# Kernel optimization log

Measured on AMD Instinct MI355X. Metric: run time of the kernel, lower is better.

The kernel has to match this reference:

```python
import jax, jax.numpy as jnp
import numpy as np
from jax import lax

EPS = 1e-5

@jax.custom_vjp
def binarize(x):
    return jnp.sign(x)

def _bin_fwd(x):
    return jnp.sign(x), x

def _bin_bwd(x, g):
    # straight-through estimator: pass grad where |x| <= 1
    return (g * (jnp.abs(x) <= 1.0).astype(g.dtype),)

binarize.defvjp(_bin_fwd, _bin_bwd)


def bconv(x, w, stride=1, pad=0):
    # BinarizeConv2d: sign-binarize both activations and weights, dense conv
    return lax.conv_general_dilated(
        binarize(x), binarize(w),
        window_strides=(stride, stride),
        padding=[(pad, pad), (pad, pad)],
        dimension_numbers=('NCHW', 'OIHW', 'NCHW'))


def bn(x, gamma, beta):
    # training-mode batch norm (grad enabled in torch forward): batch stats over (N,H,W)
    mean = x.mean(axis=(0, 2, 3), keepdims=True)
    var = ((x - mean) ** 2).mean(axis=(0, 2, 3), keepdims=True)
    return gamma * (x - mean) * lax.rsqrt(var + EPS) + beta


def hardtanh(x):
    return jnp.clip(x, -1.0, 1.0)


def setup_inputs() -> dict:
    key = jax.random.key(0)
    ks = jax.random.split(key, 4)
    N, Cin, H, W = 64, 256, 56, 56
    P = 64  # planes; expansion*planes == Cin -> identity shortcut
    return {
        'x':  jax.random.normal(ks[0], (N, Cin, H, W), dtype=jnp.float32),
        'w1': jax.random.normal(ks[1], (P, Cin, 1, 1), dtype=jnp.float32),
        'w2': jax.random.normal(ks[2], (P, P, 3, 3), dtype=jnp.float32),
        'w3': jax.random.normal(ks[3], (Cin, P, 1, 1), dtype=jnp.float32),
        'g1': jnp.ones((1, P, 1, 1), jnp.float32),
        'b1': jnp.zeros((1, P, 1, 1), jnp.float32),
        'g2': jnp.ones((1, P, 1, 1), jnp.float32),
        'b2': jnp.zeros((1, P, 1, 1), jnp.float32),
        'g3': jnp.ones((1, Cin, 1, 1), jnp.float32),
        'b3': jnp.zeros((1, Cin, 1, 1), jnp.float32),
    }


def reference(x, w1, w2, w3, g1, b1, g2, b2, g3, b3):
    out = hardtanh(bn(bconv(x, w1), g1, b1))                 # 1x1 binconv + BN + hardtanh
    out = hardtanh(bn(bconv(out, w2, stride=1, pad=1), g2, b2))  # 3x3 binconv + BN + hardtanh
    out = bn(bconv(out, w3), g3, b3)                          # 1x1 binconv + BN
    out = out + x                                             # identity shortcut
    return hardtanh(out)
```

## Files before the change

### kernel.cpp

```cpp
#include <hip/hip_runtime.h>
#include <stdint.h>
#include <math.h>

typedef unsigned long long u64;
typedef long long ll;

#define H_    56
#define W_    56
#define HW_   3136
#define N_    64
#define C_    256
#define P_    64
#define NPIX_ 200704
#define BN_EPS 1e-5

__global__ __launch_bounds__(256) void pack_weights_k(
    const float* __restrict__ w1, const float* __restrict__ w2,
    const float* __restrict__ w3,
    u64* __restrict__ ws1, u64* __restrict__ wn1,
    u64* __restrict__ ws2, u64* __restrict__ wn2, int* __restrict__ b2,
    u64* __restrict__ ws3, u64* __restrict__ wn3, int* __restrict__ b3) {
  int t = blockIdx.x * 256 + threadIdx.x;
  if (t < 64) {
    int co = t;
    for (int ch = 0; ch < 4; ++ch) {
      u64 s = 0, n = 0;
      for (int j = 0; j < 64; ++j) {
        float v = w1[co * 256 + ch * 64 + j];
        s |= ((u64)(v < 0.f)) << j;
        n |= ((u64)(v != 0.f)) << j;
      }
      ws1[co * 4 + ch] = s; wn1[co * 4 + ch] = n;
    }
  } else if (t < 64 + 576) {
    int idx = t - 64, co = idx / 9, tap = idx % 9;
    u64 s = 0, n = 0;
    for (int ci = 0; ci < 64; ++ci) {
      float v = w2[(co * 64 + ci) * 9 + tap];
      s |= ((u64)(v < 0.f)) << ci;
      n |= ((u64)(v != 0.f)) << ci;
    }
    ws2[idx] = s; wn2[idx] = n; b2[idx] = __popcll(n);
  } else if (t < 64 + 576 + 256) {
    int co = t - 640;
    u64 s = 0, n = 0;
    for (int ci = 0; ci < 64; ++ci) {
      float v = w3[co * 64 + ci];
      s |= ((u64)(v < 0.f)) << ci;
      n |= ((u64)(v != 0.f)) << ci;
    }
    ws3[co] = s; wn3[co] = n; b3[co] = __popcll(n);
  }
}

__global__ __launch_bounds__(256) void fused1_k(
    const float* __restrict__ x,
    const u64* __restrict__ ws1, const u64* __restrict__ wn1,
    short* __restrict__ y1, u64* __restrict__ gsum, u64* __restrict__ gsq) {
  __shared__ u64 lws[256], lwn[256];
  __shared__ int ssum[64], ssq[64];
  int tid = threadIdx.x;
  lws[tid] = ws1[tid]; lwn[tid] = wn1[tid];
  if (tid < 64) { ssum[tid] = 0; ssq[tid] = 0; }
  __syncthreads();

  int p = blockIdx.x * 256 + tid;
  int n = p / HW_, hw = p % HW_;
  const float* xb = x + (size_t)n * (C_ * HW_) + hw;
  u64 s[4], nb[4];
  #pragma unroll
  for (int ch = 0; ch < 4; ++ch) {
    u64 sv = 0, nv = 0;
    #pragma unroll
    for (int j = 0; j < 64; ++j) {
      float v = xb[(size_t)((ch * 64 + j) * HW_)];
      sv |= ((u64)(v < 0.f)) << j;
      nv |= ((u64)(v != 0.f)) << j;
    }
    s[ch] = sv; nb[ch] = nv;
  }

  int lane = tid & 63;
  for (int co = 0; co < 64; ++co) {
    int acc = 0;
    #pragma unroll
    for (int ch = 0; ch < 4; ++ch) {
      u64 v = nb[ch] & lwn[co * 4 + ch];
      u64 a = ~(s[ch] ^ lws[co * 4 + ch]) & v;
      acc += 2 * __popcll(a) - __popcll(v);
    }
    y1[(size_t)co * NPIX_ + p] = (short)acc;
    int rs = acc, rq = acc * acc;
    #pragma unroll
    for (int m = 32; m; m >>= 1) {
      rs += __shfl_xor(rs, m, 64);
      rq += __shfl_xor(rq, m, 64);
    }
    if (lane == 0) { atomicAdd(&ssum[co], rs); atomicAdd(&ssq[co], rq); }
  }
  __syncthreads();
  if (tid < 64) {
    atomicAdd(&gsum[tid], (u64)(ll)ssum[tid]);
    atomicAdd(&gsq[tid],  (u64)(ll)ssq[tid]);
  }
}

__global__ __launch_bounds__(256) void binpack_k(
    const short* __restrict__ y,
    const u64* __restrict__ gsum, const u64* __restrict__ gsq,
    const float* __restrict__ gamma, const float* __restrict__ beta,
    u64* __restrict__ pout) {
  __shared__ double tsc[64], tsh[64];
  int tid = threadIdx.x;
  if (tid < 64) {
    double S = (double)(ll)gsum[tid], Q = (double)(ll)gsq[tid];
    double mean = S / (double)NPIX_;
    double var  = Q / (double)NPIX_ - mean * mean;
    double inv  = 1.0 / sqrt(var + BN_EPS);
    double sc   = (double)gamma[tid] * inv;
    tsc[tid] = sc;
    tsh[tid] = (double)beta[tid] - mean * sc;
  }
  __syncthreads();
  int p = blockIdx.x * 256 + tid;
  u64 m = 0;
  #pragma unroll 8
  for (int co = 0; co < 64; ++co) {
    int v = (int)y[(size_t)co * NPIX_ + p];
    m |= ((u64)(tsc[co] * (double)v + tsh[co] < 0.0)) << co;
  }
  pout[p] = m;
}

__global__ __launch_bounds__(256) void conv2_k(
    const u64* __restrict__ p1,
    const u64* __restrict__ ws2, const u64* __restrict__ wn2,
    const int* __restrict__ b2,
    short* __restrict__ y2, u64* __restrict__ gsum, u64* __restrict__ gsq) {
  __shared__ u64 lws[576], lwn[576];
  __shared__ int lb[576];
  __shared__ int ssum[64], ssq[64];
  int tid = threadIdx.x;
  for (int j = tid; j < 576; j += 256) { lws[j] = ws2[j]; lwn[j] = wn2[j]; lb[j] = b2[j]; }
  if (tid < 64) { ssum[tid] = 0; ssq[tid] = 0; }
  __syncthreads();

  int p = blockIdx.x * 256 + tid;
  int n = p / HW_, hw = p % HW_, h = hw / W_, w = hw % W_;
  u64 tv[9]; bool ok[9];
  #pragma unroll
  for (int dh = -1; dh <= 1; ++dh)
    #pragma unroll
    for (int dw = -1; dw <= 1; ++dw) {
      int k = (dh + 1) * 3 + (dw + 1);
      int h2 = h + dh, w2c = w + dw;
      bool v = (h2 >= 0) & (h2 < H_) & (w2c >= 0) & (w2c < W_);
      ok[k] = v;
      tv[k] = v ? p1[n * HW_ + h2 * W_ + w2c] : 0ULL;
    }

  int lane = tid & 63;
  for (int co = 0; co < 64; ++co) {
    int acc = 0;
    #pragma unroll
    for (int k = 0; k < 9; ++k) {
      int wi = co * 9 + k;
      u64 a = ~(tv[k] ^ lws[wi]) & lwn[wi];
      int d = 2 * __popcll(a) - lb[wi];
      acc += ok[k] ? d : 0;
    }
    y2[(size_t)co * NPIX_ + p] = (short)acc;
    int rs = acc, rq = acc * acc;
    #pragma unroll
    for (int m = 32; m; m >>= 1) {
      rs += __shfl_xor(rs, m, 64);
      rq += __shfl_xor(rq, m, 64);
    }
    if (lane == 0) { atomicAdd(&ssum[co], rs); atomicAdd(&ssq[co], rq); }
  }
  __syncthreads();
  if (tid < 64) {
    atomicAdd(&gsum[tid], (u64)(ll)ssum[tid]);
    atomicAdd(&gsq[tid],  (u64)(ll)ssq[tid]);
  }
}

__global__ __launch_bounds__(256) void conv3_stats_k(
    const u64* __restrict__ p2,
    const u64* __restrict__ ws3, const u64* __restrict__ wn3,
    const int* __restrict__ b3,
    u64* __restrict__ gsum, u64* __restrict__ gsq) {
  int t = threadIdx.x;
  u64 s3 = ws3[t], n3 = wn3[t];
  int bb = b3[t];
  int s = 0, q = 0;
  int base = blockIdx.x * 512;
  #pragma unroll 4
  for (int i = 0; i < 512; ++i) {
    u64 m = p2[base + i];
    int yv = 2 * __popcll(~(m ^ s3) & n3) - bb;
    s += yv; q += yv * yv;
  }
  atomicAdd(&gsum[t], (u64)(ll)s);
  atomicAdd(&gsq[t],  (u64)(ll)q);
}

__global__ __launch_bounds__(256) void final_k(
    const float* __restrict__ x, const u64* __restrict__ p2,
    const u64* __restrict__ ws3, const u64* __restrict__ wn3,
    const int* __restrict__ b3,
    const u64* __restrict__ gsum, const u64* __restrict__ gsq,
    const float* __restrict__ gamma, const float* __restrict__ beta,
    float* __restrict__ out) {
  __shared__ float fsc[2], fsh[2];
  size_t base = (size_t)blockIdx.x * 1024;
  size_t r0 = base / HW_;
  if (threadIdx.x < 2) {
    int c = (int)((r0 + threadIdx.x) % C_);
    double S = (double)(ll)gsum[c], Q = (double)(ll)gsq[c];
    double mean = S / (double)NPIX_;
    double var  = Q / (double)NPIX_ - mean * mean;
    double inv  = 1.0 / sqrt(var + BN_EPS);
    double sc   = (double)gamma[c] * inv;
    fsc[threadIdx.x] = (float)sc;
    fsh[threadIdx.x] = (float)((double)beta[c] - mean * sc);
  }
  __syncthreads();

  size_t idx = base + (size_t)threadIdx.x * 4;
  size_t lin = idx / HW_;
  int rr = (int)(lin - r0);
  int co = (int)(lin % C_);
  int nn = (int)(lin / C_);
  int hw = (int)(idx % HW_);
  int pb = nn * HW_ + hw;
  u64 s3 = ws3[co], n3 = wn3[co];
  int bb = b3[co];
  float sc = fsc[rr], sh = fsh[rr];
  float4 xv = *(const float4*)(x + idx);
  float4 ov;
  int y0 = 2 * __popcll(~(p2[pb + 0] ^ s3) & n3) - bb;
  int y1 = 2 * __popcll(~(p2[pb + 1] ^ s3) & n3) - bb;
  int y2 = 2 * __popcll(~(p2[pb + 2] ^ s3) & n3) - bb;
  int y3 = 2 * __popcll(~(p2[pb + 3] ^ s3) & n3) - bb;
  ov.x = fminf(fmaxf(sc * (float)y0 + sh + xv.x, -1.f), 1.f);
  ov.y = fminf(fmaxf(sc * (float)y1 + sh + xv.y, -1.f), 1.f);
  ov.z = fminf(fmaxf(sc * (float)y2 + sh + xv.z, -1.f), 1.f);
  ov.w = fminf(fmaxf(sc * (float)y3 + sh + xv.w, -1.f), 1.f);
  *(float4*)(out + idx) = ov;
}

extern "C" void kernel_launch(void* const* d_in, const int* in_sizes, int n_in,
                              void* d_out, int out_size, void* d_ws, size_t ws_size,
                              hipStream_t stream) {
  const float* x  = (const float*)d_in[0];
  const float* w1 = (const float*)d_in[1];
  const float* w2 = (const float*)d_in[2];
  const float* w3 = (const float*)d_in[3];
  const float* g1 = (const float*)d_in[4];
  const float* b1 = (const float*)d_in[5];
  const float* g2 = (const float*)d_in[6];
  const float* b2 = (const float*)d_in[7];
  const float* g3 = (const float*)d_in[8];
  const float* b3 = (const float*)d_in[9];
  float* out = (float*)d_out;

  char* base = (char*)d_ws;
  size_t off = 0;
  auto alloc = [&](size_t bytes) -> char* {
    char* p = base + off;
    off = (off + bytes + 255) & ~(size_t)255;
    return p;
  };
  short* y1b = (short*)alloc((size_t)NPIX_ * 64 * 2);
  u64* p1   = (u64*)alloc((size_t)NPIX_ * 8);
  u64* p2   = (u64*)alloc((size_t)NPIX_ * 8);
  u64* ws1  = (u64*)alloc(256 * 8);
  u64* wn1  = (u64*)alloc(256 * 8);
  u64* ws2  = (u64*)alloc(576 * 8);
  u64* wn2  = (u64*)alloc(576 * 8);
  int* bb2  = (int*)alloc(576 * 4);
  u64* ws3  = (u64*)alloc(256 * 8);
  u64* wn3  = (u64*)alloc(256 * 8);
  int* bb3  = (int*)alloc(256 * 4);
  char* stats = alloc(768 * 8);
  u64* sum1 = (u64*)stats;          u64* sq1 = sum1 + 64;
  u64* sum2 = sq1 + 64;             u64* sq2 = sum2 + 64;
  u64* sum3 = sq2 + 64;             u64* sq3 = sum3 + 256;
  (void)ws_size; (void)n_in; (void)in_sizes; (void)out_size;

  hipMemsetAsync(stats, 0, 768 * 8, stream);

  pack_weights_k<<<4, 256, 0, stream>>>(w1, w2, w3, ws1, wn1, ws2, wn2, bb2,
                                        ws3, wn3, bb3);

  fused1_k<<<784, 256, 0, stream>>>(x, ws1, wn1, y1b, sum1, sq1);
  binpack_k<<<784, 256, 0, stream>>>(y1b, sum1, sq1, g1, b1, p1);

  conv2_k<<<784, 256, 0, stream>>>(p1, ws2, wn2, bb2, y1b, sum2, sq2);
  binpack_k<<<784, 256, 0, stream>>>(y1b, sum2, sq2, g2, b2, p2);

  conv3_stats_k<<<392, 256, 0, stream>>>(p2, ws3, wn3, bb3, sum3, sq3);

  final_k<<<50176, 256, 0, stream>>>(x, p2, ws3, wn3, bb3, sum3, sq3, g3, b3,
                                     out);
}
```

Measured before the change: 617.2 us.

## Recompute binary convs in a second pass instead of storing int16 intermediates

The first-layer sign packing is split out into its own kernel, which writes packed sign and nonzero bitplanes of x. Conv1 and conv2 now run twice: a stats-only pass, then a pass that recomputes the conv and binarizes it against an integer threshold derived from the BN stats. This removes the 25 MB short intermediate buffers and the separate binpack kernels. Threads are remapped so each lane owns an output channel with its weights held in registers, and each wave walks over pixels, building the packed words with ballots. The trade is twice the popcount work in exchange for far less memory traffic, plus a 13 MB packed-x buffer that the two conv1 passes re-read.

```diff
diff --git a/kernel.cpp b/kernel.cpp
--- a/kernel.cpp
+++ b/kernel.cpp
@@ -3,6 +3,7 @@
 #include <math.h>
 
 typedef unsigned long long u64;
+typedef unsigned int u32;
 typedef long long ll;
 
 #define H_    56
@@ -53,51 +54,87 @@
   }
 }
 
-__global__ __launch_bounds__(256) void fused1_k(
-    const float* __restrict__ x,
+__device__ inline void bn_thresh(u64 S_, u64 Q_, float g, float b,
+                                 int* A, int* X) {
+  double S = (double)(ll)S_, Q = (double)(ll)Q_;
+  double mean = S / (double)NPIX_;
+  double var  = Q / (double)NPIX_ - mean * mean;
+  double sc   = (double)g / sqrt(var + BN_EPS);
+  double sh   = (double)b - mean * sc;
+  if (sc > 0.0) {
+    double t = -sh / sc;
+    t = fmin(fmax(t, -1.0e8), 1.0e8);
+    *A = (int)ceil(t); *X = 0;
+  } else if (sc < 0.0) {
+    double t = -sh / sc;
+    t = fmin(fmax(t, -1.0e8), 1.0e8);
+    *A = (int)floor(t) + 1; *X = 1;
+  } else {
+    *A = (int)0x80000000; *X = (sh < 0.0) ? 1 : 0;
+  }
+}
+
+__global__ __launch_bounds__(64) void pack_x_k(
+    const float* __restrict__ x, u64* __restrict__ xs, u64* __restrict__ xn) {
+  int t = blockIdx.x * 64 + threadIdx.x;
+  int n = t / 784;
+  int qw = t - n * 784;
+  const float* xb = x + (size_t)n * (C_ * HW_) + qw * 4;
+  size_t p = (size_t)t * 4;
+  for (int q = 0; q < 4; ++q) {
+    u64 s0 = 0, s1 = 0, s2 = 0, s3 = 0, n0 = 0, n1 = 0, n2 = 0, n3 = 0;
+    #pragma unroll 8
+    for (int j = 0; j < 64; ++j) {
+      float4 v = *(const float4*)(xb + (size_t)(q * 64 + j) * HW_);
+      u64 bit = 1ull << j;
+      if (v.x <  0.f) s0 |= bit;
+      if (v.x != 0.f) n0 |= bit;
+      if (v.y <  0.f) s1 |= bit;
+      if (v.y != 0.f) n1 |= bit;
+      if (v.z <  0.f) s2 |= bit;
+      if (v.z != 0.f) n2 |= bit;
+      if (v.w <  0.f) s3 |= bit;
+      if (v.w != 0.f) n3 |= bit;
+    }
+    u64* os = xs + (size_t)q * NPIX_ + p;
+    u64* on = xn + (size_t)q * NPIX_ + p;
+    ulonglong2 a, b2v, c, d;
+    a.x = s0; a.y = s1; b2v.x = s2; b2v.y = s3;
+    c.x = n0; c.y = n1; d.x = n2; d.y = n3;
+    *(ulonglong2*)(os)     = a;
+    *(ulonglong2*)(os + 2) = b2v;
+    *(ulonglong2*)(on)     = c;
+    *(ulonglong2*)(on + 2) = d;
+  }
+}
+
+__global__ __launch_bounds__(256) void conv1_stats_k(
+    const u64* __restrict__ xs, const u64* __restrict__ xn,
     const u64* __restrict__ ws1, const u64* __restrict__ wn1,
-    short* __restrict__ y1, u64* __restrict__ gsum, u64* __restrict__ gsq) {
-  __shared__ u64 lws[256], lwn[256];
+    u64* __restrict__ gsum, u64* __restrict__ gsq) {
   __shared__ int ssum[64], ssq[64];
-  int tid = threadIdx.x;
-  lws[tid] = ws1[tid]; lwn[tid] = wn1[tid];
+  int tid = threadIdx.x, co = tid & 63, wv = tid >> 6;
   if (tid < 64) { ssum[tid] = 0; ssq[tid] = 0; }
+  u64 wS[4], wN[4];
+  #pragma unroll
+  for (int q = 0; q < 4; ++q) { wS[q] = ws1[co * 4 + q]; wN[q] = wn1[co * 4 + q]; }
   __syncthreads();
-
-  int p = blockIdx.x * 256 + tid;
-  int n = p / HW_, hw = p % HW_;
-  const float* xb = x + (size_t)n * (C_ * HW_) + hw;
-  u64 s[4], nb[4];
-  #pragma unroll
-  for (int ch = 0; ch < 4; ++ch) {
-    u64 sv = 0, nv = 0;
-    #pragma unroll
-    for (int j = 0; j < 64; ++j) {
-      float v = xb[(size_t)((ch * 64 + j) * HW_)];
-      sv |= ((u64)(v < 0.f)) << j;
-      nv |= ((u64)(v != 0.f)) << j;
-    }
-    s[ch] = sv; nb[ch] = nv;
-  }
-
-  int lane = tid & 63;
-  for (int co = 0; co < 64; ++co) {
+  int pbase = (blockIdx.x * 4 + wv) * 64;
+  int s = 0, qq = 0;
+  for (int i = 0; i < 64; ++i) {
+    int p = pbase + i;
     int acc = 0;
     #pragma unroll
-    for (int ch = 0; ch < 4; ++ch) {
-      u64 v = nb[ch] & lwn[co * 4 + ch];
-      u64 a = ~(s[ch] ^ lws[co * 4 + ch]) & v;
+    for (int q = 0; q < 4; ++q) {
+      u64 xv = xs[(size_t)q * NPIX_ + p];
+      u64 nv = xn[(size_t)q * NPIX_ + p];
+      u64 v = nv & wN[q];
+      u64 a = ~(xv ^ wS[q]) & v;
       acc += 2 * __popcll(a) - __popcll(v);
     }
-    y1[(size_t)co * NPIX_ + p] = (short)acc;
-    int rs = acc, rq = acc * acc;
-    #pragma unroll
-    for (int m = 32; m; m >>= 1) {
-      rs += __shfl_xor(rs, m, 64);
-      rq += __shfl_xor(rq, m, 64);
-    }
-    if (lane == 0) { atomicAdd(&ssum[co], rs); atomicAdd(&ssq[co], rq); }
-  }
+    s += acc; qq += acc * acc;
+  }
+  atomicAdd(&ssum[co], s); atomicAdd(&ssq[co], qq);
   __syncthreads();
   if (tid < 64) {
     atomicAdd(&gsum[tid], (u64)(ll)ssum[tid]);
@@ -105,84 +142,150 @@
   }
 }
 
-__global__ __launch_bounds__(256) void binpack_k(
-    const short* __restrict__ y,
+__global__ __launch_bounds__(256) void bin1_k(
+    const u64* __restrict__ xs, const u64* __restrict__ xn,
+    const u64* __restrict__ ws1, const u64* __restrict__ wn1,
     const u64* __restrict__ gsum, const u64* __restrict__ gsq,
     const float* __restrict__ gamma, const float* __restrict__ beta,
     u64* __restrict__ pout) {
-  __shared__ double tsc[64], tsh[64];
-  int tid = threadIdx.x;
-  if (tid < 64) {
-    double S = (double)(ll)gsum[tid], Q = (double)(ll)gsq[tid];
-    double mean = S / (double)NPIX_;
-    double var  = Q / (double)NPIX_ - mean * mean;
-    double inv  = 1.0 / sqrt(var + BN_EPS);
-    double sc   = (double)gamma[tid] * inv;
-    tsc[tid] = sc;
-    tsh[tid] = (double)beta[tid] - mean * sc;
-  }
-  __syncthreads();
-  int p = blockIdx.x * 256 + tid;
-  u64 m = 0;
-  #pragma unroll 8
-  for (int co = 0; co < 64; ++co) {
-    int v = (int)y[(size_t)co * NPIX_ + p];
-    m |= ((u64)(tsc[co] * (double)v + tsh[co] < 0.0)) << co;
-  }
-  pout[p] = m;
-}
-
-__global__ __launch_bounds__(256) void conv2_k(
-    const u64* __restrict__ p1,
-    const u64* __restrict__ ws2, const u64* __restrict__ wn2,
-    const int* __restrict__ b2,
-    short* __restrict__ y2, u64* __restrict__ gsum, u64* __restrict__ gsq) {
-  __shared__ u64 lws[576], lwn[576];
-  __shared__ int lb[576];
-  __shared__ int ssum[64], ssq[64];
-  int tid = threadIdx.x;
-  for (int j = tid; j < 576; j += 256) { lws[j] = ws2[j]; lwn[j] = wn2[j]; lb[j] = b2[j]; }
-  if (tid < 64) { ssum[tid] = 0; ssq[tid] = 0; }
-  __syncthreads();
-
-  int p = blockIdx.x * 256 + tid;
-  int n = p / HW_, hw = p % HW_, h = hw / W_, w = hw % W_;
-  u64 tv[9]; bool ok[9];
+  int tid = threadIdx.x, co = tid & 63, wv = tid >> 6;
+  u64 wS[4], wN[4];
   #pragma unroll
-  for (int dh = -1; dh <= 1; ++dh)
-    #pragma unroll
-    for (int dw = -1; dw <= 1; ++dw) {
-      int k = (dh + 1) * 3 + (dw + 1);
-      int h2 = h + dh, w2c = w + dw;
-      bool v = (h2 >= 0) & (h2 < H_) & (w2c >= 0) & (w2c < W_);
-      ok[k] = v;
-      tv[k] = v ? p1[n * HW_ + h2 * W_ + w2c] : 0ULL;
-    }
-
-  int lane = tid & 63;
-  for (int co = 0; co < 64; ++co) {
+  for (int q = 0; q < 4; ++q) { wS[q] = ws1[co * 4 + q]; wN[q] = wn1[co * 4 + q]; }
+  int A, X;
+  bn_thresh(gsum[co], gsq[co], gamma[co], beta[co], &A, &X);
+  int pbase = (blockIdx.x * 4 + wv) * 64;
+  u64 mw = 0;
+  for (int i = 0; i < 64; ++i) {
+    int p = pbase + i;
     int acc = 0;
     #pragma unroll
-    for (int k = 0; k < 9; ++k) {
-      int wi = co * 9 + k;
-      u64 a = ~(tv[k] ^ lws[wi]) & lwn[wi];
-      int d = 2 * __popcll(a) - lb[wi];
-      acc += ok[k] ? d : 0;
-    }
-    y2[(size_t)co * NPIX_ + p] = (short)acc;
-    int rs = acc, rq = acc * acc;
-    #pragma unroll
-    for (int m = 32; m; m >>= 1) {
-      rs += __shfl_xor(rs, m, 64);
-      rq += __shfl_xor(rq, m, 64);
-    }
-    if (lane == 0) { atomicAdd(&ssum[co], rs); atomicAdd(&ssq[co], rq); }
-  }
+    for (int q = 0; q < 4; ++q) {
+      u64 xv = xs[(size_t)q * NPIX_ + p];
+      u64 nv = xn[(size_t)q * NPIX_ + p];
+      u64 v = nv & wN[q];
+      u64 a = ~(xv ^ wS[q]) & v;
+      acc += 2 * __popcll(a) - __popcll(v);
+    }
+    u64 bal = __ballot((acc < A) ^ X);
+    mw = (co == i) ? bal : mw;
+  }
+  pout[pbase + co] = mw;
+}
+
+__device__ inline int conv2_tap(u64 t, u64 ws, u64 wn, int b) {
+  return 2 * __popcll(~(t ^ ws) & wn) - b;
+}
+
+__device__ inline int conv2_px_edge(const u64* rowp, int w, int hm, int hp,
+                                    const u64* wS, const u64* wN,
+                                    const int* wB) {
+  int wm = (w > 0), wp = (w < W_ - 1);
+  int acc = 0;
+  if (hm & wm) acc += conv2_tap(rowp[w - W_ - 1], wS[0], wN[0], wB[0]);
+  if (hm)      acc += conv2_tap(rowp[w - W_    ], wS[1], wN[1], wB[1]);
+  if (hm & wp) acc += conv2_tap(rowp[w - W_ + 1], wS[2], wN[2], wB[2]);
+  if (wm)      acc += conv2_tap(rowp[w - 1     ], wS[3], wN[3], wB[3]);
+  acc += conv2_tap(rowp[w], wS[4], wN[4], wB[4]);
+  if (wp)      acc += conv2_tap(rowp[w + 1     ], wS[5], wN[5], wB[5]);
+  if (hp & wm) acc += conv2_tap(rowp[w + W_ - 1], wS[6], wN[6], wB[6]);
+  if (hp)      acc += conv2_tap(rowp[w + W_    ], wS[7], wN[7], wB[7]);
+  if (hp & wp) acc += conv2_tap(rowp[w + W_ + 1], wS[8], wN[8], wB[8]);
+  return acc;
+}
+
+__device__ inline int conv2_px_fast(const u64* c, const u64* wS,
+                                    const u64* wN, int Bs) {
+  int P = 0;
+  P += __popcll(~(c[-W_ - 1] ^ wS[0]) & wN[0]);
+  P += __popcll(~(c[-W_    ] ^ wS[1]) & wN[1]);
+  P += __popcll(~(c[-W_ + 1] ^ wS[2]) & wN[2]);
+  P += __popcll(~(c[-1     ] ^ wS[3]) & wN[3]);
+  P += __popcll(~(c[0      ] ^ wS[4]) & wN[4]);
+  P += __popcll(~(c[1      ] ^ wS[5]) & wN[5]);
+  P += __popcll(~(c[W_ - 1 ] ^ wS[6]) & wN[6]);
+  P += __popcll(~(c[W_     ] ^ wS[7]) & wN[7]);
+  P += __popcll(~(c[W_ + 1 ] ^ wS[8]) & wN[8]);
+  return 2 * P - Bs;
+}
+
+__global__ __launch_bounds__(256) void conv2_stats_k(
+    const u64* __restrict__ p1, const u64* __restrict__ ws2,
+    const u64* __restrict__ wn2,
+    u64* __restrict__ gsum, u64* __restrict__ gsq) {
+  __shared__ int ssum[64], ssq[64];
+  int tid = threadIdx.x, co = tid & 63, wv = tid >> 6;
+  if (tid < 64) { ssum[tid] = 0; ssq[tid] = 0; }
+  u64 wS[9], wN[9]; int wB[9]; int Bs = 0;
+  #pragma unroll
+  for (int k = 0; k < 9; ++k) {
+    wS[k] = ws2[co * 9 + k]; wN[k] = wn2[co * 9 + k];
+    wB[k] = __popcll(wN[k]); Bs += wB[k];
+  }
+  __syncthreads();
+  int row = blockIdx.x * 4 + wv;
+  int n = row / H_, h = row - n * H_;
+  const u64* rowp = p1 + (size_t)n * HW_ + h * W_;
+  int hm = (h > 0), hp = (h < H_ - 1);
+  int s = 0, q = 0;
+  if (hm & hp) {
+    { int a = conv2_px_edge(rowp, 0, 1, 1, wS, wN, wB); s += a; q += a * a; }
+    for (int w = 1; w < W_ - 1; ++w) {
+      int a = conv2_px_fast(rowp + w, wS, wN, Bs);
+      s += a; q += a * a;
+    }
+    { int a = conv2_px_edge(rowp, W_ - 1, 1, 1, wS, wN, wB); s += a; q += a * a; }
+  } else {
+    for (int w = 0; w < W_; ++w) {
+      int a = conv2_px_edge(rowp, w, hm, hp, wS, wN, wB);
+      s += a; q += a * a;
+    }
+  }
+  atomicAdd(&ssum[co], s); atomicAdd(&ssq[co], q);
   __syncthreads();
   if (tid < 64) {
     atomicAdd(&gsum[tid], (u64)(ll)ssum[tid]);
     atomicAdd(&gsq[tid],  (u64)(ll)ssq[tid]);
   }
+}
+
+__global__ __launch_bounds__(256) void bin2_k(
+    const u64* __restrict__ p1, const u64* __restrict__ ws2,
+    const u64* __restrict__ wn2,
+    const u64* __restrict__ gsum, const u64* __restrict__ gsq,
+    const float* __restrict__ gamma, const float* __restrict__ beta,
+    u64* __restrict__ pout) {
+  int tid = threadIdx.x, co = tid & 63, wv = tid >> 6;
+  u64 wS[9], wN[9]; int wB[9]; int Bs = 0;
+  #pragma unroll
+  for (int k = 0; k < 9; ++k) {
+    wS[k] = ws2[co * 9 + k]; wN[k] = wn2[co * 9 + k];
+    wB[k] = __popcll(wN[k]); Bs += wB[k];
+  }
+  int A, X;
+  bn_thresh(gsum[co], gsq[co], gamma[co], beta[co], &A, &X);
+  int row = blockIdx.x * 4 + wv;
+  int n = row / H_, h = row - n * H_;
+  const u64* rowp = p1 + (size_t)n * HW_ + h * W_;
+  u64* orow = pout + (size_t)n * HW_ + h * W_;
+  int hm = (h > 0), hp = (h < H_ - 1);
+  u64 mw = 0;
+  if (hm & hp) {
+    { int a = conv2_px_edge(rowp, 0, 1, 1, wS, wN, wB);
+      u64 bal = __ballot((a < A) ^ X); mw = (co == 0) ? bal : mw; }
+    for (int w = 1; w < W_ - 1; ++w) {
+      int a = conv2_px_fast(rowp + w, wS, wN, Bs);
+      u64 bal = __ballot((a < A) ^ X); mw = (co == w) ? bal : mw;
+    }
+    { int a = conv2_px_edge(rowp, W_ - 1, 1, 1, wS, wN, wB);
+      u64 bal = __ballot((a < A) ^ X); mw = (co == W_ - 1) ? bal : mw; }
+  } else {
+    for (int w = 0; w < W_; ++w) {
+      int a = conv2_px_edge(rowp, w, hm, hp, wS, wN, wB);
+      u64 bal = __ballot((a < A) ^ X); mw = (co == w) ? bal : mw;
+    }
+  }
+  if (co < W_) orow[co] = mw;
 }
 
 __global__ __launch_bounds__(256) void conv3_stats_k(
@@ -272,7 +375,8 @@
     off = (off + bytes + 255) & ~(size_t)255;
     return p;
   };
-  short* y1b = (short*)alloc((size_t)NPIX_ * 64 * 2);
+  u64* xs   = (u64*)alloc((size_t)NPIX_ * 4 * 8);
+  u64* xnz  = (u64*)alloc((size_t)NPIX_ * 4 * 8);
   u64* p1   = (u64*)alloc((size_t)NPIX_ * 8);
   u64* p2   = (u64*)alloc((size_t)NPIX_ * 8);
   u64* ws1  = (u64*)alloc(256 * 8);
@@ -294,11 +398,13 @@
   pack_weights_k<<<4, 256, 0, stream>>>(w1, w2, w3, ws1, wn1, ws2, wn2, bb2,
                                         ws3, wn3, bb3);
 
-  fused1_k<<<784, 256, 0, stream>>>(x, ws1, wn1, y1b, sum1, sq1);
-  binpack_k<<<784, 256, 0, stream>>>(y1b, sum1, sq1, g1, b1, p1);
-
-  conv2_k<<<784, 256, 0, stream>>>(p1, ws2, wn2, bb2, y1b, sum2, sq2);
-  binpack_k<<<784, 256, 0, stream>>>(y1b, sum2, sq2, g2, b2, p2);
+  pack_x_k<<<784, 64, 0, stream>>>(x, xs, xnz);
+
+  conv1_stats_k<<<784, 256, 0, stream>>>(xs, xnz, ws1, wn1, sum1, sq1);
+  bin1_k<<<784, 256, 0, stream>>>(xs, xnz, ws1, wn1, sum1, sq1, g1, b1, p1);
+
+  conv2_stats_k<<<896, 256, 0, stream>>>(p1, ws2, wn2, sum2, sq2);
+  bin2_k<<<896, 256, 0, stream>>>(p1, ws2, wn2, sum2, sq2, g2, b2, p2);
 
   conv3_stats_k<<<392, 256, 0, stream>>>(p2, ws3, wn3, bb3, sum3, sq3);
 
```

After: 716.2 us. 16.1% more time.

## Recompute binary convs in two passes instead of storing int16 intermediates

Applied to the files above, without the earlier changes.

Packs the input sign and nonzero bitmasks once in a separate kernel. Conv1 and conv2 then each run twice: a stats pass and a recompute pass that turns the BN affine into an integer threshold and builds the packed output with wave ballots. This drops the 25 MB int16 intermediate write and reread and the separate binpack kernels. Conv2 now stages input rows in shared memory, maps threads to output channels, and special-cases the borders, while conv3 stats also stage p2 in shared memory. The cost is doing the popcount work twice and extra pack buffers.

```diff
diff --git a/kernel.cpp b/kernel.cpp
--- a/kernel.cpp
+++ b/kernel.cpp
@@ -53,135 +53,204 @@
   }
 }
 
-__global__ __launch_bounds__(256) void fused1_k(
-    const float* __restrict__ x,
+__device__ inline void bn_thresh(u64 S_, u64 Q_, float g, float b,
+                                 int* A, int* X) {
+  double S = (double)(ll)S_, Q = (double)(ll)Q_;
+  double mean = S / (double)NPIX_;
+  double var  = Q / (double)NPIX_ - mean * mean;
+  double sc   = (double)g / sqrt(var + BN_EPS);
+  double sh   = (double)b - mean * sc;
+  if (sc > 0.0) {
+    double t = -sh / sc;
+    t = fmin(fmax(t, -1.0e8), 1.0e8);
+    *A = (int)ceil(t); *X = 0;
+  } else if (sc < 0.0) {
+    double t = -sh / sc;
+    t = fmin(fmax(t, -1.0e8), 1.0e8);
+    *A = (int)floor(t) + 1; *X = 1;
+  } else {
+    *A = (int)0x80000000; *X = (sh < 0.0) ? 1 : 0;
+  }
+}
+
+__global__ __launch_bounds__(256) void pack_x_k(
+    const float* __restrict__ x, u64* __restrict__ xs, u64* __restrict__ xn) {
+  int t = blockIdx.x * 256 + threadIdx.x;
+  int n = t / 1568;
+  int pw = (t - n * 1568) * 2;
+  const float* xb = x + (size_t)n * (C_ * HW_) + pw;
+  size_t p = (size_t)t * 2;
+  for (int q = 0; q < 4; ++q) {
+    u64 s0 = 0, s1 = 0, n0 = 0, n1 = 0;
+    #pragma unroll 16
+    for (int j = 0; j < 64; ++j) {
+      float2 v = *(const float2*)(xb + (size_t)(q * 64 + j) * HW_);
+      u64 bit = 1ull << j;
+      if (v.x <  0.f) s0 |= bit;
+      if (v.x != 0.f) n0 |= bit;
+      if (v.y <  0.f) s1 |= bit;
+      if (v.y != 0.f) n1 |= bit;
+    }
+    ulonglong2 sv; sv.x = s0; sv.y = s1;
+    ulonglong2 nv; nv.x = n0; nv.y = n1;
+    *(ulonglong2*)(xs + (size_t)q * NPIX_ + p) = sv;
+    *(ulonglong2*)(xn + (size_t)q * NPIX_ + p) = nv;
+  }
+}
+
+template<int MODE>
+__global__ __launch_bounds__(256) void conv1_k(
+    const u64* __restrict__ xs, const u64* __restrict__ xn,
     const u64* __restrict__ ws1, const u64* __restrict__ wn1,
-    short* __restrict__ y1, u64* __restrict__ gsum, u64* __restrict__ gsq) {
-  __shared__ u64 lws[256], lwn[256];
+    u64* __restrict__ gsum, u64* __restrict__ gsq,
+    const float* __restrict__ gamma, const float* __restrict__ beta,
+    u64* __restrict__ pout) {
+  __shared__ ulonglong2 tile[4][256];
   __shared__ int ssum[64], ssq[64];
-  int tid = threadIdx.x;
-  lws[tid] = ws1[tid]; lwn[tid] = wn1[tid];
-  if (tid < 64) { ssum[tid] = 0; ssq[tid] = 0; }
+  int tid = threadIdx.x, co = tid & 63, wv = tid >> 6;
+  int base = blockIdx.x * 256;
+  #pragma unroll
+  for (int q = 0; q < 4; ++q) {
+    ulonglong2 v;
+    v.x = xs[(size_t)q * NPIX_ + base + tid];
+    v.y = xn[(size_t)q * NPIX_ + base + tid];
+    tile[q][tid] = v;
+  }
+  if (MODE == 0 && tid < 64) { ssum[tid] = 0; ssq[tid] = 0; }
+  u64 wS[4], wN[4];
+  #pragma unroll
+  for (int q = 0; q < 4; ++q) { wS[q] = ws1[co * 4 + q]; wN[q] = wn1[co * 4 + q]; }
+  int A = 0, X = 0;
+  if (MODE == 1) bn_thresh(gsum[co], gsq[co], gamma[co], beta[co], &A, &X);
   __syncthreads();
-
-  int p = blockIdx.x * 256 + tid;
-  int n = p / HW_, hw = p % HW_;
-  const float* xb = x + (size_t)n * (C_ * HW_) + hw;
-  u64 s[4], nb[4];
-  #pragma unroll
-  for (int ch = 0; ch < 4; ++ch) {
-    u64 sv = 0, nv = 0;
-    #pragma unroll
-    for (int j = 0; j < 64; ++j) {
-      float v = xb[(size_t)((ch * 64 + j) * HW_)];
-      sv |= ((u64)(v < 0.f)) << j;
-      nv |= ((u64)(v != 0.f)) << j;
-    }
-    s[ch] = sv; nb[ch] = nv;
-  }
-
-  int lane = tid & 63;
-  for (int co = 0; co < 64; ++co) {
+  int s = 0, qq = 0;
+  u64 mw = 0;
+  #pragma unroll 2
+  for (int i = 0; i < 64; ++i) {
+    int px = wv * 64 + i;
     int acc = 0;
     #pragma unroll
-    for (int ch = 0; ch < 4; ++ch) {
-      u64 v = nb[ch] & lwn[co * 4 + ch];
-      u64 a = ~(s[ch] ^ lws[co * 4 + ch]) & v;
+    for (int q = 0; q < 4; ++q) {
+      ulonglong2 t2 = tile[q][px];
+      u64 v = t2.y & wN[q];
+      u64 a = ~(t2.x ^ wS[q]) & v;
       acc += 2 * __popcll(a) - __popcll(v);
     }
-    y1[(size_t)co * NPIX_ + p] = (short)acc;
-    int rs = acc, rq = acc * acc;
-    #pragma unroll
-    for (int m = 32; m; m >>= 1) {
-      rs += __shfl_xor(rs, m, 64);
-      rq += __shfl_xor(rq, m, 64);
-    }
-    if (lane == 0) { atomicAdd(&ssum[co], rs); atomicAdd(&ssq[co], rq); }
-  }
-  __syncthreads();
-  if (tid < 64) {
-    atomicAdd(&gsum[tid], (u64)(ll)ssum[tid]);
-    atomicAdd(&gsq[tid],  (u64)(ll)ssq[tid]);
-  }
-}
-
-__global__ __launch_bounds__(256) void binpack_k(
-    const short* __restrict__ y,
-    const u64* __restrict__ gsum, const u64* __restrict__ gsq,
-    const float* __restrict__ gamma, const float* __restrict__ beta,
-    u64* __restrict__ pout) {
-  __shared__ double tsc[64], tsh[64];
-  int tid = threadIdx.x;
-  if (tid < 64) {
-    double S = (double)(ll)gsum[tid], Q = (double)(ll)gsq[tid];
-    double mean = S / (double)NPIX_;
-    double var  = Q / (double)NPIX_ - mean * mean;
-    double inv  = 1.0 / sqrt(var + BN_EPS);
-    double sc   = (double)gamma[tid] * inv;
-    tsc[tid] = sc;
-    tsh[tid] = (double)beta[tid] - mean * sc;
-  }
-  __syncthreads();
-  int p = blockIdx.x * 256 + tid;
-  u64 m = 0;
-  #pragma unroll 8
-  for (int co = 0; co < 64; ++co) {
-    int v = (int)y[(size_t)co * NPIX_ + p];
-    m |= ((u64)(tsc[co] * (double)v + tsh[co] < 0.0)) << co;
-  }
-  pout[p] = m;
-}
-
+    if (MODE == 0) { s += acc; qq += acc * acc; }
+    else {
+      u64 bal = __ballot((acc < A) ^ X);
+      mw = (co == i) ? bal : mw;
+    }
+  }
+  if (MODE == 0) {
+    atomicAdd(&ssum[co], s); atomicAdd(&ssq[co], qq);
+    __syncthreads();
+    if (tid < 64) {
+      atomicAdd(&gsum[tid], (u64)(ll)ssum[tid]);
+      atomicAdd(&gsq[tid],  (u64)(ll)ssq[tid]);
+    }
+  } else {
+    pout[base + wv * 64 + co] = mw;
+  }
+}
+
+__device__ inline int c2tap(u64 t, u64 ws, u64 wn) {
+  return __popcll(~(t ^ ws) & wn);
+}
+
+template<int MODE>
 __global__ __launch_bounds__(256) void conv2_k(
     const u64* __restrict__ p1,
     const u64* __restrict__ ws2, const u64* __restrict__ wn2,
-    const int* __restrict__ b2,
-    short* __restrict__ y2, u64* __restrict__ gsum, u64* __restrict__ gsq) {
-  __shared__ u64 lws[576], lwn[576];
-  __shared__ int lb[576];
+    u64* __restrict__ gsum, u64* __restrict__ gsq,
+    const float* __restrict__ gamma, const float* __restrict__ beta,
+    u64* __restrict__ pout) {
+  __shared__ u64 tile[6 * W_];
   __shared__ int ssum[64], ssq[64];
-  int tid = threadIdx.x;
-  for (int j = tid; j < 576; j += 256) { lws[j] = ws2[j]; lwn[j] = wn2[j]; lb[j] = b2[j]; }
-  if (tid < 64) { ssum[tid] = 0; ssq[tid] = 0; }
+  int tid = threadIdx.x, co = tid & 63, wv = tid >> 6;
+  int blk = blockIdx.x;
+  int n = blk / 14, t0 = blk - n * 14;
+  int h0 = t0 * 4;
+  const u64* img = p1 + (size_t)n * HW_;
+  for (int j = tid; j < 6 * W_; j += 256) {
+    int gh = h0 - 1 + j / W_;
+    int gw = j - (j / W_) * W_;
+    tile[j] = (gh >= 0 && gh < H_) ? img[gh * W_ + gw] : 0ull;
+  }
+  if (MODE == 0 && tid < 64) { ssum[tid] = 0; ssq[tid] = 0; }
+  u64 wS[9], wN[9]; int wB[9], Bs = 0;
+  #pragma unroll
+  for (int k = 0; k < 9; ++k) {
+    wS[k] = ws2[co * 9 + k]; wN[k] = wn2[co * 9 + k];
+    wB[k] = __popcll(wN[k]); Bs += wB[k];
+  }
+  int A = 0, X = 0;
+  if (MODE == 1) bn_thresh(gsum[co], gsq[co], gamma[co], beta[co], &A, &X);
   __syncthreads();
-
-  int p = blockIdx.x * 256 + tid;
-  int n = p / HW_, hw = p % HW_, h = hw / W_, w = hw % W_;
-  u64 tv[9]; bool ok[9];
-  #pragma unroll
-  for (int dh = -1; dh <= 1; ++dh)
-    #pragma unroll
-    for (int dw = -1; dw <= 1; ++dw) {
-      int k = (dh + 1) * 3 + (dw + 1);
-      int h2 = h + dh, w2c = w + dw;
-      bool v = (h2 >= 0) & (h2 < H_) & (w2c >= 0) & (w2c < W_);
-      ok[k] = v;
-      tv[k] = v ? p1[n * HW_ + h2 * W_ + w2c] : 0ULL;
-    }
-
-  int lane = tid & 63;
-  for (int co = 0; co < 64; ++co) {
-    int acc = 0;
-    #pragma unroll
-    for (int k = 0; k < 9; ++k) {
-      int wi = co * 9 + k;
-      u64 a = ~(tv[k] ^ lws[wi]) & lwn[wi];
-      int d = 2 * __popcll(a) - lb[wi];
-      acc += ok[k] ? d : 0;
-    }
-    y2[(size_t)co * NPIX_ + p] = (short)acc;
-    int rs = acc, rq = acc * acc;
-    #pragma unroll
-    for (int m = 32; m; m >>= 1) {
-      rs += __shfl_xor(rs, m, 64);
-      rq += __shfl_xor(rq, m, 64);
-    }
-    if (lane == 0) { atomicAdd(&ssum[co], rs); atomicAdd(&ssq[co], rq); }
-  }
-  __syncthreads();
-  if (tid < 64) {
-    atomicAdd(&gsum[tid], (u64)(ll)ssum[tid]);
-    atomicAdd(&gsq[tid],  (u64)(ll)ssq[tid]);
+  int h = h0 + wv;
+  const u64* rA = tile + wv * W_;
+  const u64* rB = rA + W_;
+  const u64* rC = rB + W_;
+  int vA = (h > 0), vC = (h < H_ - 1);
+  int s = 0, qq = 0;
+  u64 mw = 0;
+  if (vA & vC) {
+    {
+      int P = c2tap(rA[0], wS[1], wN[1]) + c2tap(rA[1], wS[2], wN[2])
+            + c2tap(rB[0], wS[4], wN[4]) + c2tap(rB[1], wS[5], wN[5])
+            + c2tap(rC[0], wS[7], wN[7]) + c2tap(rC[1], wS[8], wN[8]);
+      int acc = 2 * P - (wB[1] + wB[2] + wB[4] + wB[5] + wB[7] + wB[8]);
+      if (MODE == 0) { s += acc; qq += acc * acc; }
+      else { u64 bal = __ballot((acc < A) ^ X); mw = (co == 0) ? bal : mw; }
+    }
+    #pragma unroll 2
+    for (int w = 1; w < W_ - 1; ++w) {
+      int P = c2tap(rA[w-1], wS[0], wN[0]) + c2tap(rA[w], wS[1], wN[1]) + c2tap(rA[w+1], wS[2], wN[2])
+            + c2tap(rB[w-1], wS[3], wN[3]) + c2tap(rB[w], wS[4], wN[4]) + c2tap(rB[w+1], wS[5], wN[5])
+            + c2tap(rC[w-1], wS[6], wN[6]) + c2tap(rC[w], wS[7], wN[7]) + c2tap(rC[w+1], wS[8], wN[8]);
+      int acc = 2 * P - Bs;
+      if (MODE == 0) { s += acc; qq += acc * acc; }
+      else { u64 bal = __ballot((acc < A) ^ X); mw = (co == w) ? bal : mw; }
+    }
+    {
+      int P = c2tap(rA[W_-2], wS[0], wN[0]) + c2tap(rA[W_-1], wS[1], wN[1])
+            + c2tap(rB[W_-2], wS[3], wN[3]) + c2tap(rB[W_-1], wS[4], wN[4])
+            + c2tap(rC[W_-2], wS[6], wN[6]) + c2tap(rC[W_-1], wS[7], wN[7]);
+      int acc = 2 * P - (wB[0] + wB[1] + wB[3] + wB[4] + wB[6] + wB[7]);
+      if (MODE == 0) { s += acc; qq += acc * acc; }
+      else { u64 bal = __ballot((acc < A) ^ X); mw = (co == W_ - 1) ? bal : mw; }
+    }
+  } else {
+    for (int w = 0; w < W_; ++w) {
+      int wm = w > 0, wp = w < W_ - 1;
+      int P = 0, B = 0;
+      if (vA) {
+        if (wm) { P += c2tap(rA[w-1], wS[0], wN[0]); B += wB[0]; }
+        P += c2tap(rA[w], wS[1], wN[1]); B += wB[1];
+        if (wp) { P += c2tap(rA[w+1], wS[2], wN[2]); B += wB[2]; }
+      }
+      if (wm) { P += c2tap(rB[w-1], wS[3], wN[3]); B += wB[3]; }
+      P += c2tap(rB[w], wS[4], wN[4]); B += wB[4];
+      if (wp) { P += c2tap(rB[w+1], wS[5], wN[5]); B += wB[5]; }
+      if (vC) {
+        if (wm) { P += c2tap(rC[w-1], wS[6], wN[6]); B += wB[6]; }
+        P += c2tap(rC[w], wS[7], wN[7]); B += wB[7];
+        if (wp) { P += c2tap(rC[w+1], wS[8], wN[8]); B += wB[8]; }
+      }
+      int acc = 2 * P - B;
+      if (MODE == 0) { s += acc; qq += acc * acc; }
+      else { u64 bal = __ballot((acc < A) ^ X); mw = (co == w) ? bal : mw; }
+    }
+  }
+  if (MODE == 0) {
+    atomicAdd(&ssum[co], s); atomicAdd(&ssq[co], qq);
+    __syncthreads();
+    if (tid < 64) {
+      atomicAdd(&gsum[tid], (u64)(ll)ssum[tid]);
+      atomicAdd(&gsq[tid],  (u64)(ll)ssq[tid]);
+    }
+  } else {
+    if (co < W_) pout[(size_t)n * HW_ + h * W_ + co] = mw;
   }
 }
 
@@ -190,15 +259,17 @@
     const u64* __restrict__ ws3, const u64* __restrict__ wn3,
     const int* __restrict__ b3,
     u64* __restrict__ gsum, u64* __restrict__ gsq) {
+  __shared__ u64 tile[512];
   int t = threadIdx.x;
+  int base = blockIdx.x * 512;
+  *(ulonglong2*)&tile[t * 2] = *(const ulonglong2*)&p2[base + t * 2];
   u64 s3 = ws3[t], n3 = wn3[t];
   int bb = b3[t];
+  __syncthreads();
   int s = 0, q = 0;
-  int base = blockIdx.x * 512;
   #pragma unroll 4
   for (int i = 0; i < 512; ++i) {
-    u64 m = p2[base + i];
-    int yv = 2 * __popcll(~(m ^ s3) & n3) - bb;
+    int yv = 2 * __popcll(~(tile[i] ^ s3) & n3) - bb;
     s += yv; q += yv * yv;
   }
   atomicAdd(&gsum[t], (u64)(ll)s);
@@ -272,7 +343,8 @@
     off = (off + bytes + 255) & ~(size_t)255;
     return p;
   };
-  short* y1b = (short*)alloc((size_t)NPIX_ * 64 * 2);
+  u64* xs   = (u64*)alloc((size_t)NPIX_ * 4 * 8);
+  u64* xnz  = (u64*)alloc((size_t)NPIX_ * 4 * 8);
   u64* p1   = (u64*)alloc((size_t)NPIX_ * 8);
   u64* p2   = (u64*)alloc((size_t)NPIX_ * 8);
   u64* ws1  = (u64*)alloc(256 * 8);
@@ -294,11 +366,17 @@
   pack_weights_k<<<4, 256, 0, stream>>>(w1, w2, w3, ws1, wn1, ws2, wn2, bb2,
                                         ws3, wn3, bb3);
 
-  fused1_k<<<784, 256, 0, stream>>>(x, ws1, wn1, y1b, sum1, sq1);
-  binpack_k<<<784, 256, 0, stream>>>(y1b, sum1, sq1, g1, b1, p1);
-
-  conv2_k<<<784, 256, 0, stream>>>(p1, ws2, wn2, bb2, y1b, sum2, sq2);
-  binpack_k<<<784, 256, 0, stream>>>(y1b, sum2, sq2, g2, b2, p2);
+  pack_x_k<<<392, 256, 0, stream>>>(x, xs, xnz);
+
+  conv1_k<0><<<784, 256, 0, stream>>>(xs, xnz, ws1, wn1, sum1, sq1,
+                                      g1, b1, (u64*)nullptr);
+  conv1_k<1><<<784, 256, 0, stream>>>(xs, xnz, ws1, wn1, sum1, sq1,
+                                      g1, b1, p1);
+
+  conv2_k<0><<<896, 256, 0, stream>>>(p1, ws2, wn2, sum2, sq2,
+                                      g2, b2, (u64*)nullptr);
+  conv2_k<1><<<896, 256, 0, stream>>>(p1, ws2, wn2, sum2, sq2,
+                                      g2, b2, p2);
 
   conv3_stats_k<<<392, 256, 0, stream>>>(p2, ws3, wn3, bb3, sum3, sq3);
 
```

New measurement: 589.7 us. 4.5% less time.
